# Optimization experiments

Measured on AMD Instinct MI355X. Metric: run time of the kernel, lower is better.

## Reference

```python
import jax, jax.numpy as jnp
import numpy as np

B, S, D, H = 2, 4096, 1024, 16
HD = D // H  # 64
BASE = 10000.0


def setup_inputs() -> dict:
    key = jax.random.key(0)
    ks = jax.random.split(key, 11)
    s = 1.0 / np.sqrt(D)
    return {
        "consulta": jax.random.normal(ks[0], (B, S, D), jnp.float32),
        "chave": jax.random.normal(ks[1], (B, S, D), jnp.float32),
        "valor": jax.random.normal(ks[2], (B, S, D), jnp.float32),
        "Wq": jax.random.normal(ks[3], (D, D), jnp.float32) * s,
        "bq": jnp.zeros((D,), jnp.float32),
        "Wk": jax.random.normal(ks[4], (D, D), jnp.float32) * s,
        "bk": jnp.zeros((D,), jnp.float32),
        "Wv": jax.random.normal(ks[5], (D, D), jnp.float32) * s,
        "bv": jnp.zeros((D,), jnp.float32),
        "Wo": jax.random.normal(ks[6], (D, D), jnp.float32) * s,
        "bo": jnp.zeros((D,), jnp.float32),
    }


def _rope(x):
    # x: [B, H, S, HD]; rotate interleaved (even, odd) pairs
    seq = x.shape[2]
    theta = 1.0 / (BASE ** (jnp.arange(0, HD, 2, dtype=jnp.float32) / HD))  # [HD/2]
    angles = jnp.arange(seq, dtype=jnp.float32)[:, None] * theta[None, :]  # [S, HD/2]
    cos, sin = jnp.cos(angles), jnp.sin(angles)
    xr = x.reshape(*x.shape[:-1], HD // 2, 2)
    x_re, x_im = xr[..., 0], xr[..., 1]
    out_re = x_re * cos - x_im * sin
    out_im = x_re * sin + x_im * cos
    return jnp.stack([out_re, out_im], axis=-1).reshape(x.shape)


def reference(consulta, chave, valor, Wq, bq, Wk, bk, Wv, bv, Wo, bo):
    b, s, _ = consulta.shape
    # projections (torch Linear: x @ W.T + b)
    Q = consulta @ Wq.T + bq
    K = chave @ Wk.T + bk
    V = valor @ Wv.T + bv
    # [B, H, S, HD]
    Q = Q.reshape(b, s, H, HD).transpose(0, 2, 1, 3)
    K = K.reshape(b, s, H, HD).transpose(0, 2, 1, 3)
    V = V.reshape(b, s, H, HD).transpose(0, 2, 1, 3)
    Q = _rope(Q)
    K = _rope(K)
    scores = jnp.einsum('bhqd,bhkd->bhqk', Q, K) / jnp.sqrt(jnp.float32(HD))
    weights = jax.nn.softmax(scores, axis=-1)  # dropout p=0 -> identity
    out = jnp.einsum('bhqk,bhkd->bhqd', weights, V)
    out = out.transpose(0, 2, 1, 3).reshape(b, s, D)
    return out @ Wo.T + bo
```

## Files before the change

kernel.cpp:

```cpp
#include <hip/hip_runtime.h>
#include <hip/hip_bf16.h>

typedef __attribute__((ext_vector_type(8))) short short8;
typedef __attribute__((ext_vector_type(4))) float f32x4;
typedef __attribute__((ext_vector_type(16))) float f32x16;
typedef __attribute__((ext_vector_type(4))) unsigned short ushort4v;
typedef __attribute__((ext_vector_type(4))) float float4v;
typedef __attribute__((ext_vector_type(2))) unsigned int uint32x2;
typedef __attribute__((ext_vector_type(4))) unsigned int uint32x4;

#define NB 2
#define NS 4096
#define ND 1024
#define NH 16
#define NHD 64

#define QSCALE 0.18033688011112042f

__device__ __forceinline__ unsigned short f2bf(float x) {
    union { float f; unsigned u; } v; v.f = x;
    unsigned r = v.u + 0x7FFFu + ((v.u >> 16) & 1u);
    return (unsigned short)(r >> 16);
}

__device__ __forceinline__ unsigned cvt_pk_bf16(float lo, float hi) {
    unsigned r;
    asm("v_cvt_pk_bf16_f32 %0, %1, %2" : "=v"(r) : "v"(lo), "v"(hi));
    return r;
}

__device__ __forceinline__ void gload_lds16(const unsigned short* g, unsigned short* l) {
    __builtin_amdgcn_global_load_lds(
        (const __attribute__((address_space(1))) void*)g,
        (__attribute__((address_space(3))) void*)l,
        16, 0, 0);
}

__global__ void rope_table_kernel(float* __restrict__ cosT, float* __restrict__ sinT) {
    int i = blockIdx.x * blockDim.x + threadIdx.x;
    int p = i & 31, s = i >> 5;
    float theta = exp2f(-(float)(2 * p) * (13.287712379549449f / 64.0f));
    float ang = (float)s * theta;
    float sv, cv;
    sincosf(ang, &sv, &cv);
    cosT[i] = cv; sinT[i] = sv;
}

__global__ void cast_bf16_kernel(const float* __restrict__ in, unsigned short* __restrict__ out, int n8) {
    int i = blockIdx.x * blockDim.x + threadIdx.x;
    if (i >= n8) return;
    float4v a0 = *(const float4v*)(&in[(size_t)i * 8]);
    float4v a1 = *(const float4v*)(&in[(size_t)i * 8 + 4]);
    short8 s8;
    s8[0] = (short)f2bf(a0.x); s8[1] = (short)f2bf(a0.y);
    s8[2] = (short)f2bf(a0.z); s8[3] = (short)f2bf(a0.w);
    s8[4] = (short)f2bf(a1.x); s8[5] = (short)f2bf(a1.y);
    s8[6] = (short)f2bf(a1.z); s8[7] = (short)f2bf(a1.w);
    *(short8*)(&out[(size_t)i * 8]) = s8;
}

__global__ __launch_bounds__(256, 3) void gemm_qkv_kernel(
    const unsigned short* __restrict__ A0,
    const unsigned short* __restrict__ A1,
    const unsigned short* __restrict__ A2,
    const unsigned short* __restrict__ W3,
    const float* __restrict__ biasq,
    const float* __restrict__ biask,
    const float* __restrict__ biasv,
    unsigned short* __restrict__ Qrb,
    unsigned short* __restrict__ Krb,
    unsigned short* __restrict__ Vtb,
    const float* __restrict__ cosT,
    const float* __restrict__ sinT,
    int which_base)
{
    __shared__ unsigned short As[128 * 32];
    __shared__ unsigned short Bs[128 * 32];
    const int t = threadIdx.x;
    const int wave = t >> 6, lane = t & 63;
    const int quad = lane >> 4, l15 = lane & 15;
    const int wm = (wave & 1) * 64, wn = (wave >> 1) * 64;
    const int m0 = blockIdx.y * 128;
    const int n0g = blockIdx.x * 128;
    const int which = (n0g >> 10) + which_base;
    const int n0 = n0g & 1023;
    const unsigned short* A = (which == 0) ? A0 : (which == 1) ? A1 : A2;

    f32x4 acc[4][4];
#pragma unroll
    for (int i = 0; i < 4; i++)
#pragma unroll
        for (int j = 0; j < 4; j++)
            acc[i][j] = f32x4{0.f, 0.f, 0.f, 0.f};

    for (int k0 = 0; k0 < ND; k0 += 32) {
#pragma unroll
        for (int p = 0; p < 2; p++) {
            int idx = p * 256 + t;
            int r = idx >> 2, c = (idx & 3) * 8;
            unsigned short* ldsA = &As[(size_t)(p * 256 + wave * 64) * 8];
            unsigned short* ldsB = &Bs[(size_t)(p * 256 + wave * 64) * 8];
            gload_lds16(&A[(size_t)(m0 + r) * ND + k0 + c], ldsA);
            gload_lds16(&W3[(size_t)(n0g + r) * ND + k0 + c], ldsB);
        }
        __syncthreads();

        short8 af[4], bfr[4];
#pragma unroll
        for (int mt = 0; mt < 4; mt++)
            af[mt] = *(const short8*)(&As[(wm + mt * 16 + l15) * 32 + quad * 8]);
#pragma unroll
        for (int nt = 0; nt < 4; nt++)
            bfr[nt] = *(const short8*)(&Bs[(wn + nt * 16 + l15) * 32 + quad * 8]);
#pragma unroll
        for (int mt = 0; mt < 4; mt++)
#pragma unroll
            for (int nt = 0; nt < 4; nt++)
                acc[mt][nt] = __builtin_amdgcn_mfma_f32_16x16x32_bf16(af[mt], bfr[nt], acc[mt][nt], 0, 0, 0);
        __syncthreads();
    }

    if (which < 2) {
        unsigned short* out = (which == 0) ? Qrb : Krb;
        const float* bias = (which == 0) ? biasq : biask;
        const float oscale = (which == 0) ? QSCALE : 1.0f;
#pragma unroll
        for (int nt = 0; nt < 4; nt++) {
            int gn = n0 + wn + nt * 16 + l15;
            int h = gn >> 6, hd = gn & 63, pr = hd >> 1, im = gn & 1;
            float bvv = bias[gn];
#pragma unroll
            for (int mt = 0; mt < 4; mt++) {
                int gm0 = m0 + wm + mt * 16 + quad * 4;
#pragma unroll
                for (int r = 0; r < 4; r++) {
                    int gm = gm0 + r;
                    int b = gm >> 12, s = gm & 4095;
                    float v = acc[mt][nt][r] + bvv;
                    float pv = __shfl_xor(v, 1, 64);
                    float cv = cosT[s * 32 + pr], sv = sinT[s * 32 + pr];
                    float o = im ? (pv * sv + v * cv) : (v * cv - pv * sv);
                    out[((size_t)(b * NH + h) * NS + s) * NHD + hd] = f2bf(o * oscale);
                }
            }
        }
    } else {
#pragma unroll
        for (int nt = 0; nt < 4; nt++) {
            int gn = n0 + wn + nt * 16 + l15;
            int h = gn >> 6, hd = gn & 63;
            float bvv = biasv[gn];
#pragma unroll
            for (int mt = 0; mt < 4; mt++) {
                int gm0 = m0 + wm + mt * 16 + quad * 4;
                int b = gm0 >> 12, s0 = gm0 & 4095;
                ushort4v pk;
#pragma unroll
                for (int r = 0; r < 4; r++)
                    pk[r] = f2bf(acc[mt][nt][r] + bvv);
                *(ushort4v*)(&Vtb[((size_t)(b * NH + h) * NHD + hd) * NS + s0]) = pk;
            }
        }
    }
}

__global__ __launch_bounds__(256, 2) void gemm_o_kernel(
    const unsigned short* __restrict__ A,
    const unsigned short* __restrict__ Wb,
    const float* __restrict__ bias,
    float* __restrict__ out)
{
    __shared__ unsigned short As[128 * 32];
    __shared__ unsigned short Bs[128 * 32];
    const int t = threadIdx.x;
    const int wave = t >> 6, lane = t & 63;
    const int quad = lane >> 4, l15 = lane & 15;
    const int wm = (wave & 1) * 64, wn = (wave >> 1) * 64;
    const int m0 = blockIdx.y * 128, n0 = blockIdx.x * 128;

    f32x4 acc[4][4];
#pragma unroll
    for (int i = 0; i < 4; i++)
#pragma unroll
        for (int j = 0; j < 4; j++)
            acc[i][j] = f32x4{0.f, 0.f, 0.f, 0.f};

    for (int k0 = 0; k0 < ND; k0 += 32) {
#pragma unroll
        for (int p = 0; p < 2; p++) {
            int idx = p * 256 + t;
            int r = idx >> 2, c = (idx & 3) * 8;
            unsigned short* ldsA = &As[(size_t)(p * 256 + wave * 64) * 8];
            unsigned short* ldsB = &Bs[(size_t)(p * 256 + wave * 64) * 8];
            gload_lds16(&A[(size_t)(m0 + r) * ND + k0 + c], ldsA);
            gload_lds16(&Wb[(size_t)(n0 + r) * ND + k0 + c], ldsB);
        }
        __syncthreads();

        short8 af[4], bfr[4];
#pragma unroll
        for (int mt = 0; mt < 4; mt++)
            af[mt] = *(const short8*)(&As[(wm + mt * 16 + l15) * 32 + quad * 8]);
#pragma unroll
        for (int nt = 0; nt < 4; nt++)
            bfr[nt] = *(const short8*)(&Bs[(wn + nt * 16 + l15) * 32 + quad * 8]);
#pragma unroll
        for (int mt = 0; mt < 4; mt++)
#pragma unroll
            for (int nt = 0; nt < 4; nt++)
                acc[mt][nt] = __builtin_amdgcn_mfma_f32_16x16x32_bf16(bfr[nt], af[mt], acc[mt][nt], 0, 0, 0);
        __syncthreads();
    }

#pragma unroll
    for (int mt = 0; mt < 4; mt++) {
        int gm = m0 + wm + mt * 16 + l15;
#pragma unroll
        for (int nt = 0; nt < 4; nt++) {
            int gn0 = n0 + wn + nt * 16 + quad * 4;
            float4v fv;
#pragma unroll
            for (int r = 0; r < 4; r++)
                fv[r] = acc[mt][nt][r] + bias[gn0 + r];
            *(float4v*)(&out[(size_t)gm * ND + gn0]) = fv;
        }
    }
}

__global__ __launch_bounds__(256, 2) void flash_kernel(
    const unsigned short* __restrict__ Qr,
    const unsigned short* __restrict__ Kr,
    const unsigned short* __restrict__ Vt,
    unsigned short* __restrict__ Yatt)
{
    __shared__ unsigned short Ks[128 * 72];
    __shared__ unsigned short Vs[64 * 136];
    const int t = threadIdx.x;
    const int wave = t >> 6, lane = t & 63;
    const int l31 = lane & 31, h = lane >> 5;
    const int bh = blockIdx.y;
    const int qb = blockIdx.x * 128;
    const int wq = wave * 32;
    const size_t base = (size_t)bh * NS * NHD;

    short8 qf[4];
#pragma unroll
    for (int ks = 0; ks < 4; ks++)
        qf[ks] = *(const short8*)(&Qr[base + (size_t)(qb + wq + l31) * NHD + ks * 16 + h * 8]);

    f32x16 zacc;
#pragma unroll
    for (int r = 0; r < 16; r++)
        zacc[r] = 0.f;

    f32x16 accO[2];
    accO[0] = zacc; accO[1] = zacc;
    float mrow = -1e30f, lrow = 0.f;

    for (int j0 = 0; j0 < NS; j0 += 128) {
#pragma unroll
        for (int p = 0; p < 4; p++) {
            int idx = p * 256 + t;
            { int r = idx >> 3, c = (idx & 7) * 8;
              *(short8*)(&Ks[r * 72 + c]) = *(const short8*)(&Kr[base + (size_t)(j0 + r) * NHD + c]); }
            { int r = idx >> 4, c = (idx & 15) * 8;
              *(short8*)(&Vs[r * 136 + c]) = *(const short8*)(&Vt[(size_t)(bh * NHD + r) * NS + j0 + c]); }
        }
        __syncthreads();

        f32x16 sa[4];
        __builtin_amdgcn_s_setprio(1);
#pragma unroll
        for (int kt = 0; kt < 4; kt++) {
            short8 ak0 = *(const short8*)(&Ks[(kt * 32 + l31) * 72 + h * 8]);
            f32x16 s = __builtin_amdgcn_mfma_f32_32x32x16_bf16(ak0, qf[0], zacc, 0, 0, 0);
#pragma unroll
            for (int ks = 1; ks < 4; ks++) {
                short8 ak = *(const short8*)(&Ks[(kt * 32 + l31) * 72 + ks * 16 + h * 8]);
                s = __builtin_amdgcn_mfma_f32_32x32x16_bf16(ak, qf[ks], s, 0, 0, 0);
            }
            sa[kt] = s;
        }
        __builtin_amdgcn_s_setprio(0);

        float mx = -1e30f;
#pragma unroll
        for (int kt = 0; kt < 4; kt++) {
            float m0v = fmaxf(fmaxf(sa[kt][0], sa[kt][1]), fmaxf(sa[kt][2], sa[kt][3]));
            float m1v = fmaxf(fmaxf(sa[kt][4], sa[kt][5]), fmaxf(sa[kt][6], sa[kt][7]));
            float m2v = fmaxf(fmaxf(sa[kt][8], sa[kt][9]), fmaxf(sa[kt][10], sa[kt][11]));
            float m3v = fmaxf(fmaxf(sa[kt][12], sa[kt][13]), fmaxf(sa[kt][14], sa[kt][15]));
            mx = fmaxf(mx, fmaxf(fmaxf(m0v, m1v), fmaxf(m2v, m3v)));
        }
        mx = fmaxf(mx, __shfl_xor(mx, 32, 64));
        if (!__all(mx <= mrow + 8.0f)) {
            float mnew = fmaxf(mrow, mx);
            float alpha = exp2f(mrow - mnew);
            lrow *= alpha;
#pragma unroll
            for (int dt = 0; dt < 2; dt++)
#pragma unroll
                for (int r = 0; r < 16; r++)
                    accO[dt][r] *= alpha;
            mrow = mnew;
        }
        float ls0 = 0.f, ls1 = 0.f, ls2 = 0.f, ls3 = 0.f;
        unsigned pk[4][4][2];
#pragma unroll
        for (int kt = 0; kt < 4; kt++)
#pragma unroll
            for (int g = 0; g < 4; g++) {
                float p0 = exp2f(sa[kt][4 * g + 0] - mrow);
                float p1 = exp2f(sa[kt][4 * g + 1] - mrow);
                float p2 = exp2f(sa[kt][4 * g + 2] - mrow);
                float p3 = exp2f(sa[kt][4 * g + 3] - mrow);
                ls0 += p0; ls1 += p1; ls2 += p2; ls3 += p3;
                pk[kt][g][0] = cvt_pk_bf16(p0, p1);
                pk[kt][g][1] = cvt_pk_bf16(p2, p3);
            }
        float lsum = (ls0 + ls1) + (ls2 + ls3);
        lsum += __shfl_xor(lsum, 32, 64);
        lrow += lsum;

#pragma unroll
        for (int t2 = 0; t2 < 4; t2++)
#pragma unroll
            for (int u = 0; u < 2; u++)
#pragma unroll
                for (int j = 0; j < 2; j++)
                    asm volatile("v_permlane32_swap_b32 %0, %1"
                                 : "+v"(pk[t2][2 * u][j]), "+v"(pk[t2][2 * u + 1][j]));

        __builtin_amdgcn_s_setprio(1);
#pragma unroll
        for (int ks2 = 0; ks2 < 8; ks2++) {
            const int t2 = ks2 >> 1, u = ks2 & 1;
            uint32x4 bw;
            bw.x = pk[t2][2 * u][0];     bw.y = pk[t2][2 * u][1];
            bw.z = pk[t2][2 * u + 1][0]; bw.w = pk[t2][2 * u + 1][1];
            short8 bp = __builtin_bit_cast(short8, bw);
#pragma unroll
            for (int dt = 0; dt < 2; dt++) {
                short8 av = *(const short8*)(&Vs[(dt * 32 + l31) * 136 + ks2 * 16 + h * 8]);
                accO[dt] = __builtin_amdgcn_mfma_f32_32x32x16_bf16(av, bp, accO[dt], 0, 0, 0);
            }
        }
        __builtin_amdgcn_s_setprio(0);
        __syncthreads();
    }

    int b = bh >> 4, hh = bh & 15;
    float rl = 1.f / lrow;
    int s = qb + wq + l31;
#pragma unroll
    for (int dt = 0; dt < 2; dt++)
#pragma unroll
        for (int g = 0; g < 4; g++) {
            uint32x2 w;
            w.x = cvt_pk_bf16(accO[dt][4 * g + 0] * rl, accO[dt][4 * g + 1] * rl);
            w.y = cvt_pk_bf16(accO[dt][4 * g + 2] * rl, accO[dt][4 * g + 3] * rl);
            int d0 = dt * 32 + 8 * g + 4 * h;
            *(uint32x2*)(&Yatt[((size_t)(b * NS + s)) * ND + hh * NHD + d0]) = w;
        }
}

extern "C" void kernel_launch(void* const* d_in, const int* in_sizes, int n_in,
                              void* d_out, int out_size, void* d_ws, size_t ws_size,
                              hipStream_t stream) {
    const float* consulta = (const float*)d_in[0];
    const float* chave    = (const float*)d_in[1];
    const float* valor    = (const float*)d_in[2];
    const float* Wq = (const float*)d_in[3];
    const float* bq = (const float*)d_in[4];
    const float* Wk = (const float*)d_in[5];
    const float* bk = (const float*)d_in[6];
    const float* Wv = (const float*)d_in[7];
    const float* bv = (const float*)d_in[8];
    const float* Wo = (const float*)d_in[9];
    const float* bo = (const float*)d_in[10];

    const size_t NX = (size_t)8192 * 1024;
    const size_t NW = (size_t)ND * ND;

    const int ACT8 = (int)(NX / 8);
    const int W8 = (int)(NW / 8);

    float* cosT = (float*)d_ws;
    float* sinT = cosT + (size_t)NS * 32;
    unsigned short* Qrb = (unsigned short*)(sinT + (size_t)NS * 32);
    unsigned short* Krb = Qrb + NX;
    unsigned short* Vtb = Krb + NX;
    unsigned short* Yat = Vtb + NX;
    unsigned short* A0  = Yat + NX;

    const size_t need_merged =
        (size_t)NS * 32 * 2 * sizeof(float) + (4 + 3) * NX * 2 + 3 * NW * 2;
    const bool merged = ws_size >= need_merged;

    rope_table_kernel<<<NS * 32 / 256, 256, 0, stream>>>(cosT, sinT);

    if (merged) {
        unsigned short* A1 = A0 + NX;
        unsigned short* A2 = A1 + NX;
        unsigned short* W3 = A2 + NX;

        cast_bf16_kernel<<<ACT8 / 256, 256, 0, stream>>>(consulta, A0, ACT8);
        cast_bf16_kernel<<<ACT8 / 256, 256, 0, stream>>>(chave,    A1, ACT8);
        cast_bf16_kernel<<<ACT8 / 256, 256, 0, stream>>>(valor,    A2, ACT8);
        cast_bf16_kernel<<<W8 / 256, 256, 0, stream>>>(Wq, W3,          W8);
        cast_bf16_kernel<<<W8 / 256, 256, 0, stream>>>(Wk, W3 + NW,     W8);
        cast_bf16_kernel<<<W8 / 256, 256, 0, stream>>>(Wv, W3 + 2 * NW, W8);

        gemm_qkv_kernel<<<dim3(24, 64), 256, 0, stream>>>(
            A0, A1, A2, W3, bq, bk, bv, Qrb, Krb, Vtb, cosT, sinT, 0);

        flash_kernel<<<dim3(32, 32), 256, 0, stream>>>(Qrb, Krb, Vtb, Yat);

        cast_bf16_kernel<<<W8 / 256, 256, 0, stream>>>(Wo, W3, W8);
        gemm_o_kernel<<<dim3(8, 64), 256, 0, stream>>>(Yat, W3, bo, (float*)d_out);
    } else {
        unsigned short* W3 = A0 + NX;

        const float* acts[3]  = {consulta, chave, valor};
        const float* ws[3]    = {Wq, Wk, Wv};
        for (int i = 0; i < 3; i++) {
            cast_bf16_kernel<<<ACT8 / 256, 256, 0, stream>>>(acts[i], A0, ACT8);
            cast_bf16_kernel<<<W8 / 256, 256, 0, stream>>>(ws[i], W3, W8);
            gemm_qkv_kernel<<<dim3(8, 64), 256, 0, stream>>>(
                A0, A0, A0, W3, bq, bk, bv, Qrb, Krb, Vtb, cosT, sinT, i);
        }

        flash_kernel<<<dim3(32, 32), 256, 0, stream>>>(Qrb, Krb, Vtb, Yat);

        cast_bf16_kernel<<<W8 / 256, 256, 0, stream>>>(Wo, W3, W8);
        gemm_o_kernel<<<dim3(8, 64), 256, 0, stream>>>(Yat, W3, bo, (float*)d_out);
    }
}
```

Baseline: 524.4 us.

## Double-buffer LDS tiles and remap workgroups in QKV and output GEMMs

Both projection GEMMs now keep two LDS buffers and issue the global-to-LDS loads for the next K-slice before computing on the current one. This hides load latency behind the MFMA work and drops one barrier per iteration. Workgroup IDs are also remapped with a stride-8 swizzle, likely so that tiles sharing inputs land on the same XCD/L2. The QKV kernel's occupancy hint drops from 3 to 2 to make room for the doubled LDS.

```diff
diff --git a/kernel.cpp b/kernel.cpp
--- a/kernel.cpp
+++ b/kernel.cpp
@@ -59,7 +59,7 @@
     *(short8*)(&out[(size_t)i * 8]) = s8;
 }
 
-__global__ __launch_bounds__(256, 3) void gemm_qkv_kernel(
+__global__ __launch_bounds__(256, 2) void gemm_qkv_kernel(
     const unsigned short* __restrict__ A0,
     const unsigned short* __restrict__ A1,
     const unsigned short* __restrict__ A2,
@@ -74,14 +74,21 @@
     const float* __restrict__ sinT,
     int which_base)
 {
-    __shared__ unsigned short As[128 * 32];
-    __shared__ unsigned short Bs[128 * 32];
+    __shared__ unsigned short As[2][128 * 32];
+    __shared__ unsigned short Bs[2][128 * 32];
     const int t = threadIdx.x;
     const int wave = t >> 6, lane = t & 63;
     const int quad = lane >> 4, l15 = lane & 15;
     const int wm = (wave & 1) * 64, wn = (wave >> 1) * 64;
-    const int m0 = blockIdx.y * 128;
-    const int n0g = blockIdx.x * 128;
+
+    const int gx = gridDim.x;
+    const int nwg = gx * gridDim.y;
+    const int flat = blockIdx.y * gx + blockIdx.x;
+    const int nf = (flat & 7) * (nwg >> 3) + (flat >> 3);
+    const int bx = nf % gx, by = nf / gx;
+
+    const int m0 = by * 128;
+    const int n0g = bx * 128;
     const int which = (n0g >> 10) + which_base;
     const int n0 = n0g & 1023;
     const unsigned short* A = (which == 0) ? A0 : (which == 1) ? A1 : A2;
@@ -93,31 +100,43 @@
         for (int j = 0; j < 4; j++)
             acc[i][j] = f32x4{0.f, 0.f, 0.f, 0.f};
 
+#pragma unroll
+    for (int p = 0; p < 2; p++) {
+        int idx = p * 256 + t;
+        int r = idx >> 2, c = (idx & 3) * 8;
+        gload_lds16(&A[(size_t)(m0 + r) * ND + c], &As[0][(p * 256 + wave * 64) * 8]);
+        gload_lds16(&W3[(size_t)(n0g + r) * ND + c], &Bs[0][(p * 256 + wave * 64) * 8]);
+    }
+    __syncthreads();
+
+    int cur = 0;
     for (int k0 = 0; k0 < ND; k0 += 32) {
-#pragma unroll
-        for (int p = 0; p < 2; p++) {
-            int idx = p * 256 + t;
-            int r = idx >> 2, c = (idx & 3) * 8;
-            unsigned short* ldsA = &As[(size_t)(p * 256 + wave * 64) * 8];
-            unsigned short* ldsB = &Bs[(size_t)(p * 256 + wave * 64) * 8];
-            gload_lds16(&A[(size_t)(m0 + r) * ND + k0 + c], ldsA);
-            gload_lds16(&W3[(size_t)(n0g + r) * ND + k0 + c], ldsB);
-        }
-        __syncthreads();
+        if (k0 + 32 < ND) {
+            int nb = cur ^ 1, k1 = k0 + 32;
+#pragma unroll
+            for (int p = 0; p < 2; p++) {
+                int idx = p * 256 + t;
+                int r = idx >> 2, c = (idx & 3) * 8;
+                gload_lds16(&A[(size_t)(m0 + r) * ND + k1 + c], &As[nb][(p * 256 + wave * 64) * 8]);
+                gload_lds16(&W3[(size_t)(n0g + r) * ND + k1 + c], &Bs[nb][(p * 256 + wave * 64) * 8]);
+            }
+        }
 
         short8 af[4], bfr[4];
 #pragma unroll
         for (int mt = 0; mt < 4; mt++)
-            af[mt] = *(const short8*)(&As[(wm + mt * 16 + l15) * 32 + quad * 8]);
+            af[mt] = *(const short8*)(&As[cur][(wm + mt * 16 + l15) * 32 + quad * 8]);
 #pragma unroll
         for (int nt = 0; nt < 4; nt++)
-            bfr[nt] = *(const short8*)(&Bs[(wn + nt * 16 + l15) * 32 + quad * 8]);
+            bfr[nt] = *(const short8*)(&Bs[cur][(wn + nt * 16 + l15) * 32 + quad * 8]);
 #pragma unroll
         for (int mt = 0; mt < 4; mt++)
 #pragma unroll
             for (int nt = 0; nt < 4; nt++)
                 acc[mt][nt] = __builtin_amdgcn_mfma_f32_16x16x32_bf16(af[mt], bfr[nt], acc[mt][nt], 0, 0, 0);
+
         __syncthreads();
+        cur ^= 1;
     }
 
     if (which < 2) {
@@ -170,13 +189,19 @@
     const float* __restrict__ bias,
     float* __restrict__ out)
 {
-    __shared__ unsigned short As[128 * 32];
-    __shared__ unsigned short Bs[128 * 32];
+    __shared__ unsigned short As[2][128 * 32];
+    __shared__ unsigned short Bs[2][128 * 32];
     const int t = threadIdx.x;
     const int wave = t >> 6, lane = t & 63;
     const int quad = lane >> 4, l15 = lane & 15;
     const int wm = (wave & 1) * 64, wn = (wave >> 1) * 64;
-    const int m0 = blockIdx.y * 128, n0 = blockIdx.x * 128;
+
+    const int gx = gridDim.x;
+    const int nwg = gx * gridDim.y;
+    const int flat = blockIdx.y * gx + blockIdx.x;
+    const int nf = (flat & 7) * (nwg >> 3) + (flat >> 3);
+    const int bx = nf % gx, by = nf / gx;
+    const int m0 = by * 128, n0 = bx * 128;
 
     f32x4 acc[4][4];
 #pragma unroll
@@ -185,31 +210,43 @@
         for (int j = 0; j < 4; j++)
             acc[i][j] = f32x4{0.f, 0.f, 0.f, 0.f};
 
+#pragma unroll
+    for (int p = 0; p < 2; p++) {
+        int idx = p * 256 + t;
+        int r = idx >> 2, c = (idx & 3) * 8;
+        gload_lds16(&A[(size_t)(m0 + r) * ND + c], &As[0][(p * 256 + wave * 64) * 8]);
+        gload_lds16(&Wb[(size_t)(n0 + r) * ND + c], &Bs[0][(p * 256 + wave * 64) * 8]);
+    }
+    __syncthreads();
+
+    int cur = 0;
     for (int k0 = 0; k0 < ND; k0 += 32) {
-#pragma unroll
-        for (int p = 0; p < 2; p++) {
-            int idx = p * 256 + t;
-            int r = idx >> 2, c = (idx & 3) * 8;
-            unsigned short* ldsA = &As[(size_t)(p * 256 + wave * 64) * 8];
-            unsigned short* ldsB = &Bs[(size_t)(p * 256 + wave * 64) * 8];
-            gload_lds16(&A[(size_t)(m0 + r) * ND + k0 + c], ldsA);
-            gload_lds16(&Wb[(size_t)(n0 + r) * ND + k0 + c], ldsB);
-        }
-        __syncthreads();
+        if (k0 + 32 < ND) {
+            int nb = cur ^ 1, k1 = k0 + 32;
+#pragma unroll
+            for (int p = 0; p < 2; p++) {
+                int idx = p * 256 + t;
+                int r = idx >> 2, c = (idx & 3) * 8;
+                gload_lds16(&A[(size_t)(m0 + r) * ND + k1 + c], &As[nb][(p * 256 + wave * 64) * 8]);
+                gload_lds16(&Wb[(size_t)(n0 + r) * ND + k1 + c], &Bs[nb][(p * 256 + wave * 64) * 8]);
+            }
+        }
 
         short8 af[4], bfr[4];
 #pragma unroll
         for (int mt = 0; mt < 4; mt++)
-            af[mt] = *(const short8*)(&As[(wm + mt * 16 + l15) * 32 + quad * 8]);
+            af[mt] = *(const short8*)(&As[cur][(wm + mt * 16 + l15) * 32 + quad * 8]);
 #pragma unroll
         for (int nt = 0; nt < 4; nt++)
-            bfr[nt] = *(const short8*)(&Bs[(wn + nt * 16 + l15) * 32 + quad * 8]);
+            bfr[nt] = *(const short8*)(&Bs[cur][(wn + nt * 16 + l15) * 32 + quad * 8]);
 #pragma unroll
         for (int mt = 0; mt < 4; mt++)
 #pragma unroll
             for (int nt = 0; nt < 4; nt++)
                 acc[mt][nt] = __builtin_amdgcn_mfma_f32_16x16x32_bf16(bfr[nt], af[mt], acc[mt][nt], 0, 0, 0);
+
         __syncthreads();
+        cur ^= 1;
     }
 
 #pragma unroll
```

New measurement: 506.7 us. -3.4%, faster.
